# Kernel tuning notes

Hardware: AMD Instinct MI355X
Metric: run time of the kernel (lower is better)

The kernel has to match this reference:

```python
import jax, jax.numpy as jnp
import numpy as np

K = 32
START = K - 2  # index of <START>
STOP = K - 1   # index of <STOP>
NEG = -10000.0
B, T = 512, 2048


def setup_inputs() -> dict:
    key = jax.random.key(0)
    k1, k2, k3, k4 = jax.random.split(key, 4)
    feats = jax.random.normal(k1, (B, T, K), dtype=jnp.float32)
    transitions = jax.random.normal(k2, (K, K), dtype=jnp.float32)
    # constraints set in __init__: never transition TO START, never FROM STOP
    transitions = transitions.at[START, :].set(NEG).at[:, STOP].set(NEG)
    tags = jax.random.randint(k3, (B, T), 0, K - 2)          # real tags only
    lens = jnp.maximum(jax.random.randint(k4, (B,), 0, T), 1)  # at least 1 token
    return {"feats": feats, "transitions": transitions, "tags": tags, "lens": lens}


def _crf_loss(feats, transitions, tags, lens):
    Bn, Tn, Kn = feats.shape
    # ---- forward algorithm (log-partition) ----
    init = jnp.full((Bn, Kn), NEG, feats.dtype).at[:, START].set(0.0)

    def step(alpha, emit):
        # alpha[b,prev] + trans[next,prev] -> logsumexp over prev, then + emit[b,next]
        nxt = jax.scipy.special.logsumexp(
            alpha[:, None, :] + transitions[None, :, :], axis=2) + emit
        return nxt, nxt

    _, alphas = jax.lax.scan(step, init, jnp.swapaxes(feats, 0, 1))  # [T,B,K]
    alphas = jnp.concatenate([init[None], alphas], axis=0)           # [T+1,B,K]
    alpha_at_len = alphas[lens, jnp.arange(Bn)]                      # [B,K]
    forward_score = jax.scipy.special.logsumexp(
        alpha_at_len + transitions[STOP][None, :], axis=1)           # [B]

    # ---- gold score ----
    tags_stop = jnp.where(jnp.arange(Tn)[None, :] < lens[:, None], tags, STOP)
    pad_start = jnp.concatenate(
        [jnp.full((Bn, 1), START, tags.dtype), tags], axis=1)        # [B,T+1]
    pad_stop = jnp.concatenate(
        [tags_stop, jnp.full((Bn, 1), STOP, tags.dtype)], axis=1)    # [B,T+1]
    trans_mask = jnp.arange(Tn + 1)[None, :] <= lens[:, None]        # len+1 transitions
    trans_sc = jnp.where(trans_mask, transitions[pad_stop, pad_start], 0.0).sum(axis=1)
    emit_mask = jnp.arange(Tn)[None, :] < lens[:, None]
    emit_sc = jnp.where(
        emit_mask,
        jnp.take_along_axis(feats, tags[:, :, None], axis=2)[..., 0],
        0.0).sum(axis=1)
    gold_score = trans_sc + emit_sc

    return jnp.mean(forward_score - gold_score)


def reference(feats, transitions, tags, lens):
    return _crf_loss(feats, transitions, tags, lens)
```

## Files before the change

kernel.cpp:

```cpp
#include <hip/hip_runtime.h>
#include <hip/hip_bf16.h>
#include <cstdint>
#include <cstddef>

#define Kn 32
#define Bn 512
#define Tn 2048
#define CH 128
#define NC (Tn / CH)
#define GP 4
#define MMB (Bn * 2)
#define GB  Bn
#define START 30
#define STOP 31
#define LN2F 0.69314718055994530942f

typedef __attribute__((ext_vector_type(8))) short bf16x8;
typedef __attribute__((ext_vector_type(16))) float f32x16;
typedef __attribute__((ext_vector_type(2))) float f32x2;

union BF8 { bf16x8 v; unsigned u[4]; };

__device__ __forceinline__ unsigned pk2z(float lo, float hi) {
  return __builtin_amdgcn_perm(__float_as_uint(hi), __float_as_uint(lo),
                               0x07060302u);
}

__device__ __forceinline__ float bcast32(float v, int idx) {
  return __shfl(v, idx, 32);
}

__global__ __launch_bounds__(256, 4) void crf_fused(
    const float* __restrict__ feats, const float* __restrict__ trans,
    const int* __restrict__ tags, const int* __restrict__ lens,
    float* __restrict__ pmats, float* __restrict__ poffs,
    float* __restrict__ gold_part) {
  const int wid = threadIdx.x >> 6;
  const int lane = threadIdx.x & 63;

  if (blockIdx.x < MMB) {
    const int b = blockIdx.x >> 1;
    const int widx = (blockIdx.x & 1) * 4 + wid;
    const int len = lens[b];
    const int m = lane & 31;
    const int h = lane >> 5;

    f32x2 e1[4], e2[4];
    {
      const float* tr = trans + m * Kn + 8 * h;
#pragma unroll
      for (int j = 0; j < 4; ++j) {
        e1[j] = (f32x2){__expf(tr[2 * j]) * 0.0078125f,
                        __expf(tr[2 * j + 1]) * 0.0078125f};
        e2[j] = (f32x2){__expf(tr[16 + 2 * j]) * 0.0078125f,
                        __expf(tr[16 + 2 * j + 1]) * 0.0078125f};
      }
    }
    unsigned i1[4] = {0, 0, 0, 0}, i2[4] = {0, 0, 0, 0};
    {
      int j = m - 8 * h;
      if (0 <= j && j < 8) i1[j >> 1] = (j & 1) ? 0x3F800000u : 0x00003F80u;
      j = m - 16 - 8 * h;
      if (0 <= j && j < 8) i2[j >> 1] = (j & 1) ? 0x3F800000u : 0x00003F80u;
    }
    const f32x16 zf = {0.f, 0.f, 0.f, 0.f, 0.f, 0.f, 0.f, 0.f,
                       0.f, 0.f, 0.f, 0.f, 0.f, 0.f, 0.f, 0.f};

    for (int cc = 0; cc < 2; ++cc) {
      const int c = widx + cc * 8;
      const int nsteps = min(max(len - c * CH, 0), CH);
      if (nsteps == 0) break;

      unsigned b1u[4], b2u[4];
#pragma unroll
      for (int j = 0; j < 4; ++j) { b1u[j] = i1[j]; b2u[j] = i2[j]; }

      f32x16 acc;
      float off = 0.0f;
      const int t0 = c * CH;
      const float* fb = feats + ((size_t)b * Tn + t0) * Kn + m;
      const int lim = Tn - 1 - t0;

      float ring[8];
#pragma unroll
      for (int i = 0; i < 8; ++i) ring[i] = fb[(size_t)min(i, lim) * Kn];

      auto mmstep = [&](float f, bool rn) {
        const float w = __expf(f);
        const f32x2 w2 = {w, w};
        BF8 A1, A2, B1, B2;
#pragma unroll
        for (int j = 0; j < 4; ++j) {
          const f32x2 p1 = e1[j] * w2;
          const f32x2 p2 = e2[j] * w2;
          A1.u[j] = pk2z(p1.x, p1.y);
          A2.u[j] = pk2z(p2.x, p2.y);
          B1.u[j] = b1u[j];
          B2.u[j] = b2u[j];
        }
        acc = __builtin_amdgcn_mfma_f32_32x32x16_bf16(A2.v, B2.v, zf, 0, 0, 0);
        acc = __builtin_amdgcn_mfma_f32_32x32x16_bf16(A1.v, B1.v, acc, 0, 0, 0);

        if (rn) {
          float mx = acc[0];
#pragma unroll
          for (int r = 1; r < 16; ++r) mx = fmaxf(mx, acc[r]);
#pragma unroll
          for (int d = 1; d < 64; d <<= 1) mx = fmaxf(mx, __shfl_xor(mx, d));
          const int e = (int)((__float_as_uint(mx) >> 23) & 255u);
          const float sc = __uint_as_float((unsigned)(254 - e) << 23);
#pragma unroll
          for (int r = 0; r < 16; ++r) acc[r] *= sc;
          off += (float)(e - 127) * LN2F;
        }

        const unsigned qa = pk2z(acc[0], acc[1]);
        const unsigned qb = pk2z(acc[2], acc[3]);
        const unsigned qc = pk2z(acc[4], acc[5]);
        const unsigned qd = pk2z(acc[6], acc[7]);
        const unsigned qe = pk2z(acc[8], acc[9]);
        const unsigned qf = pk2z(acc[10], acc[11]);
        const unsigned qg = pk2z(acc[12], acc[13]);
        const unsigned qh = pk2z(acc[14], acc[15]);
        const unsigned ra = __shfl_xor(qa, 32);
        const unsigned rb = __shfl_xor(qb, 32);
        const unsigned rc = __shfl_xor(qc, 32);
        const unsigned rd = __shfl_xor(qd, 32);
        const unsigned re = __shfl_xor(qe, 32);
        const unsigned rf = __shfl_xor(qf, 32);
        const unsigned rg = __shfl_xor(qg, 32);
        const unsigned rh = __shfl_xor(qh, 32);
        b1u[0] = h ? rc : qa;
        b1u[1] = h ? rd : qb;
        b1u[2] = h ? qc : ra;
        b1u[3] = h ? qd : rb;
        b2u[0] = h ? rg : qe;
        b2u[1] = h ? rh : qf;
        b2u[2] = h ? qg : re;
        b2u[3] = h ? qh : rf;
      };

      int t = 0;
      const int nb = nsteps >> 3;
      for (int mb = 0; mb < nb; ++mb) {
#pragma unroll
        for (int i = 0; i < 8; ++i) {
          const float f = ring[i];
          ring[i] = fb[(size_t)min(t + i + 8, lim) * Kn];
          mmstep(f, ((t + i) & 31) == 31);
        }
        t += 8;
      }
      const int rem = nsteps & 7;
      for (int i = 0; i < rem; ++i) mmstep(ring[i], false);

      float* pm = pmats + (size_t)(b * NC + c) * (Kn * Kn);
#pragma unroll
      for (int r = 0; r < 16; ++r) {
        const int row = (r & 3) + 8 * (r >> 2) + 4 * h;
        pm[row * Kn + m] = acc[r];
      }
      if (lane == 0) poffs[b * NC + c] = off + 7.0f * LN2F * (float)nsteps;
    }
  } else {
    const int b = blockIdx.x - MMB;
    const int len = lens[b];
    const int* tg = tags + (size_t)b * Tn;
    const float* fbp = feats + (size_t)b * Tn * Kn;
    float acc = 0.f;
    for (int tt = 64 * wid + lane; tt < len; tt += 256) {
      const int tag = tg[tt];
      const int prev = tt ? tg[tt - 1] : START;
      acc += fbp[(size_t)tt * Kn + tag] + trans[tag * Kn + prev];
      if (tt == len - 1) acc += trans[STOP * Kn + tag];
    }
#pragma unroll
    for (int msk = 32; msk >= 1; msk >>= 1) acc += __shfl_xor(acc, msk);
    if (lane == 0) gold_part[b * GP + wid] = acc;
  }
}

__device__ __forceinline__ float renorm_s(float& s, float off) {
  int e = (int)((__float_as_uint(s) >> 23) & 255u);
  e = max(e, __shfl_xor(e, 1));
  e = max(e, __shfl_xor(e, 2));
  e = max(e, __shfl_xor(e, 4));
  e = max(e, __shfl_xor(e, 8));
  e = max(e, __shfl_xor(e, 16));
  s *= __uint_as_float((unsigned)(254 - e) << 23);
  return off + (float)(e - 127) * LN2F;
}

__global__ __launch_bounds__(64, 1) void crf_apply(
    const float* __restrict__ trans, const int* __restrict__ lens,
    const float* __restrict__ pmats, const float* __restrict__ poffs,
    const float* __restrict__ gold_part, float* __restrict__ out) {
  const int lane = threadIdx.x;
  const int b = blockIdx.x;
  const int n = lane & 31;
  const int hb = (lane >> 5) * 16;
  const int len = lens[b];
  const int nc = (len + CH - 1) / CH;
  float s = (n == START) ? 1.0f : 0.0f;
  float off = 0.0f;
  for (int c = 0; c < nc; ++c) {
    const float* pm = pmats + (size_t)(b * NC + c) * (Kn * Kn) + n * Kn + hb;
    const float4 p0 = *(const float4*)pm;
    const float4 p1 = *(const float4*)(pm + 4);
    const float4 p2 = *(const float4*)(pm + 8);
    const float4 p3 = *(const float4*)(pm + 12);
    float a0 = 0.f, a1 = 0.f, a2 = 0.f, a3 = 0.f;
    a0 = fmaf(bcast32(s, hb + 0), p0.x, a0);
    a0 = fmaf(bcast32(s, hb + 1), p0.y, a0);
    a0 = fmaf(bcast32(s, hb + 2), p0.z, a0);
    a0 = fmaf(bcast32(s, hb + 3), p0.w, a0);
    a1 = fmaf(bcast32(s, hb + 4), p1.x, a1);
    a1 = fmaf(bcast32(s, hb + 5), p1.y, a1);
    a1 = fmaf(bcast32(s, hb + 6), p1.z, a1);
    a1 = fmaf(bcast32(s, hb + 7), p1.w, a1);
    a2 = fmaf(bcast32(s, hb + 8), p2.x, a2);
    a2 = fmaf(bcast32(s, hb + 9), p2.y, a2);
    a2 = fmaf(bcast32(s, hb + 10), p2.z, a2);
    a2 = fmaf(bcast32(s, hb + 11), p2.w, a2);
    a3 = fmaf(bcast32(s, hb + 12), p3.x, a3);
    a3 = fmaf(bcast32(s, hb + 13), p3.y, a3);
    a3 = fmaf(bcast32(s, hb + 14), p3.z, a3);
    a3 = fmaf(bcast32(s, hb + 15), p3.w, a3);
    float p = (a0 + a1) + (a2 + a3);
    p += __shfl_xor(p, 32);
    s = p;
    off = renorm_s(s, off);
    off += poffs[b * NC + c];
  }
  const float es = __expf(trans[STOP * Kn + n]);
  float q = s * es;
#pragma unroll
  for (int d = 1; d < 32; d <<= 1) q += __shfl_xor(q, d);
  if (lane == 0) {
    const float fs = __logf(q) + off;
    float gs = 0.f;
#pragma unroll
    for (int p = 0; p < GP; ++p) gs += gold_part[b * GP + p];
    atomicAdd(out, (fs - gs) * (1.0f / (float)Bn));
  }
}

extern "C" void kernel_launch(void* const* d_in, const int* in_sizes, int n_in,
                              void* d_out, int out_size, void* d_ws, size_t ws_size,
                              hipStream_t stream) {
  const float* feats = (const float*)d_in[0];
  const float* trans = (const float*)d_in[1];
  const int* tags = (const int*)d_in[2];
  const int* lens = (const int*)d_in[3];

  float* gold_part = (float*)d_ws;
  float* poffs = gold_part + (size_t)Bn * GP;
  float* pmats = poffs + (size_t)Bn * NC;

  hipMemsetAsync(d_out, 0, (size_t)out_size * sizeof(float), stream);
  crf_fused<<<MMB + GB, 256, 0, stream>>>(feats, trans, tags, lens, pmats,
                                          poffs, gold_part);
  crf_apply<<<Bn, 64, 0, stream>>>(trans, lens, pmats, poffs, gold_part,
                                   (float*)d_out);
}
```

Baseline: 282.3 us.

## Interleave two adjacent chunk chains per wave and stage apply matrices in LDS

Each wave now processes two adjacent chunks (c0, c1) at once instead of two widely spaced chunks in sequence. Their MFMA dependency chains are interleaved so one chain's latency can hide the other's. Waves whose chunks lie entirely past the sequence length now exit early. The cross-half shuffles are replaced with v_permlane32_swap, and occupancy is lowered to 3 blocks to make room for the extra registers. The apply kernel now uses 256 threads to cooperatively load all chunk matrices into swizzled shared memory before a single wave runs the serial chain. This takes global-load latency off that serial chain, at the cost of a barrier and more LDS.

```diff
diff --git a/kernel.cpp b/kernel.cpp
--- a/kernel.cpp
+++ b/kernel.cpp
@@ -1,5 +1,4 @@
 #include <hip/hip_runtime.h>
-#include <hip/hip_bf16.h>
 #include <cstdint>
 #include <cstddef>
 
@@ -30,7 +29,20 @@
   return __shfl(v, idx, 32);
 }
 
-__global__ __launch_bounds__(256, 4) void crf_fused(
+__device__ __forceinline__ void plswap(unsigned& a, unsigned& b) {
+  asm("v_permlane32_swap_b32 %0, %1" : "+v"(a), "+v"(b));
+}
+
+struct Chain {
+  unsigned bu[8];
+  f32x16 acc;
+  float off;
+  float ring[8];
+  const float* fb;
+  int lim;
+};
+
+__global__ __launch_bounds__(256, 3) void crf_fused(
     const float* __restrict__ feats, const float* __restrict__ trans,
     const int* __restrict__ tags, const int* __restrict__ lens,
     float* __restrict__ pmats, float* __restrict__ poffs,
@@ -42,6 +54,11 @@
     const int b = blockIdx.x >> 1;
     const int widx = (blockIdx.x & 1) * 4 + wid;
     const int len = lens[b];
+    const int c0 = 2 * widx, c1 = c0 + 1;
+    const int n0 = min(max(len - c0 * CH, 0), CH);
+    const int n1 = min(max(len - c1 * CH, 0), CH);
+    if (n0 == 0) return;
+
     const int m = lane & 31;
     const int h = lane >> 5;
 
@@ -56,111 +73,122 @@
                         __expf(tr[16 + 2 * j + 1]) * 0.0078125f};
       }
     }
-    unsigned i1[4] = {0, 0, 0, 0}, i2[4] = {0, 0, 0, 0};
-    {
+    const f32x16 zf = {0.f, 0.f, 0.f, 0.f, 0.f, 0.f, 0.f, 0.f,
+                       0.f, 0.f, 0.f, 0.f, 0.f, 0.f, 0.f, 0.f};
+
+    auto init_chain = [&](Chain& ch, int c) {
+      unsigned i1[4] = {0, 0, 0, 0}, i2[4] = {0, 0, 0, 0};
       int j = m - 8 * h;
       if (0 <= j && j < 8) i1[j >> 1] = (j & 1) ? 0x3F800000u : 0x00003F80u;
       j = m - 16 - 8 * h;
       if (0 <= j && j < 8) i2[j >> 1] = (j & 1) ? 0x3F800000u : 0x00003F80u;
-    }
-    const f32x16 zf = {0.f, 0.f, 0.f, 0.f, 0.f, 0.f, 0.f, 0.f,
-                       0.f, 0.f, 0.f, 0.f, 0.f, 0.f, 0.f, 0.f};
-
-    for (int cc = 0; cc < 2; ++cc) {
-      const int c = widx + cc * 8;
-      const int nsteps = min(max(len - c * CH, 0), CH);
-      if (nsteps == 0) break;
-
-      unsigned b1u[4], b2u[4];
-#pragma unroll
-      for (int j = 0; j < 4; ++j) { b1u[j] = i1[j]; b2u[j] = i2[j]; }
-
-      f32x16 acc;
-      float off = 0.0f;
+#pragma unroll
+      for (int k = 0; k < 4; ++k) { ch.bu[k] = i1[k]; ch.bu[4 + k] = i2[k]; }
+      ch.off = 0.f;
       const int t0 = c * CH;
-      const float* fb = feats + ((size_t)b * Tn + t0) * Kn + m;
-      const int lim = Tn - 1 - t0;
-
-      float ring[8];
-#pragma unroll
-      for (int i = 0; i < 8; ++i) ring[i] = fb[(size_t)min(i, lim) * Kn];
-
-      auto mmstep = [&](float f, bool rn) {
-        const float w = __expf(f);
-        const f32x2 w2 = {w, w};
-        BF8 A1, A2, B1, B2;
-#pragma unroll
-        for (int j = 0; j < 4; ++j) {
-          const f32x2 p1 = e1[j] * w2;
-          const f32x2 p2 = e2[j] * w2;
-          A1.u[j] = pk2z(p1.x, p1.y);
-          A2.u[j] = pk2z(p2.x, p2.y);
-          B1.u[j] = b1u[j];
-          B2.u[j] = b2u[j];
-        }
-        acc = __builtin_amdgcn_mfma_f32_32x32x16_bf16(A2.v, B2.v, zf, 0, 0, 0);
-        acc = __builtin_amdgcn_mfma_f32_32x32x16_bf16(A1.v, B1.v, acc, 0, 0, 0);
-
-        if (rn) {
-          float mx = acc[0];
-#pragma unroll
-          for (int r = 1; r < 16; ++r) mx = fmaxf(mx, acc[r]);
-#pragma unroll
-          for (int d = 1; d < 64; d <<= 1) mx = fmaxf(mx, __shfl_xor(mx, d));
-          const int e = (int)((__float_as_uint(mx) >> 23) & 255u);
-          const float sc = __uint_as_float((unsigned)(254 - e) << 23);
-#pragma unroll
-          for (int r = 0; r < 16; ++r) acc[r] *= sc;
-          off += (float)(e - 127) * LN2F;
-        }
-
-        const unsigned qa = pk2z(acc[0], acc[1]);
-        const unsigned qb = pk2z(acc[2], acc[3]);
-        const unsigned qc = pk2z(acc[4], acc[5]);
-        const unsigned qd = pk2z(acc[6], acc[7]);
-        const unsigned qe = pk2z(acc[8], acc[9]);
-        const unsigned qf = pk2z(acc[10], acc[11]);
-        const unsigned qg = pk2z(acc[12], acc[13]);
-        const unsigned qh = pk2z(acc[14], acc[15]);
-        const unsigned ra = __shfl_xor(qa, 32);
-        const unsigned rb = __shfl_xor(qb, 32);
-        const unsigned rc = __shfl_xor(qc, 32);
-        const unsigned rd = __shfl_xor(qd, 32);
-        const unsigned re = __shfl_xor(qe, 32);
-        const unsigned rf = __shfl_xor(qf, 32);
-        const unsigned rg = __shfl_xor(qg, 32);
-        const unsigned rh = __shfl_xor(qh, 32);
-        b1u[0] = h ? rc : qa;
-        b1u[1] = h ? rd : qb;
-        b1u[2] = h ? qc : ra;
-        b1u[3] = h ? qd : rb;
-        b2u[0] = h ? rg : qe;
-        b2u[1] = h ? rh : qf;
-        b2u[2] = h ? qg : re;
-        b2u[3] = h ? qh : rf;
-      };
-
-      int t = 0;
-      const int nb = nsteps >> 3;
-      for (int mb = 0; mb < nb; ++mb) {
-#pragma unroll
-        for (int i = 0; i < 8; ++i) {
-          const float f = ring[i];
-          ring[i] = fb[(size_t)min(t + i + 8, lim) * Kn];
-          mmstep(f, ((t + i) & 31) == 31);
-        }
-        t += 8;
-      }
-      const int rem = nsteps & 7;
-      for (int i = 0; i < rem; ++i) mmstep(ring[i], false);
-
-      float* pm = pmats + (size_t)(b * NC + c) * (Kn * Kn);
+      ch.fb = feats + ((size_t)b * Tn + t0) * Kn + m;
+      ch.lim = Tn - 1 - t0;
+#pragma unroll
+      for (int i = 0; i < 8; ++i) ch.ring[i] = ch.fb[(size_t)min(i, ch.lim) * Kn];
+    };
+
+    auto mm = [&](Chain& ch, float f, bool rn) {
+      const float w = __expf(f);
+      const f32x2 w2 = {w, w};
+      BF8 A1, A2, B1, B2;
+#pragma unroll
+      for (int j = 0; j < 4; ++j) {
+        const f32x2 p1 = e1[j] * w2;
+        const f32x2 p2 = e2[j] * w2;
+        A1.u[j] = pk2z(p1.x, p1.y);
+        A2.u[j] = pk2z(p2.x, p2.y);
+        B1.u[j] = ch.bu[j];
+        B2.u[j] = ch.bu[4 + j];
+      }
+      f32x16 acc = __builtin_amdgcn_mfma_f32_32x32x16_bf16(A2.v, B2.v, zf, 0, 0, 0);
+      acc = __builtin_amdgcn_mfma_f32_32x32x16_bf16(A1.v, B1.v, acc, 0, 0, 0);
+
+      if (rn) {
+        float mx = acc[0];
+#pragma unroll
+        for (int r = 1; r < 16; ++r) mx = fmaxf(mx, acc[r]);
+#pragma unroll
+        for (int d = 1; d < 64; d <<= 1) mx = fmaxf(mx, __shfl_xor(mx, d));
+        const int e = (int)((__float_as_uint(mx) >> 23) & 255u);
+        const float sc = __uint_as_float((unsigned)(254 - e) << 23);
+#pragma unroll
+        for (int r = 0; r < 16; ++r) acc[r] *= sc;
+        ch.off += (float)(e - 127) * LN2F;
+      }
+
+      unsigned qa = pk2z(acc[0], acc[1]);
+      unsigned qb = pk2z(acc[2], acc[3]);
+      unsigned qc = pk2z(acc[4], acc[5]);
+      unsigned qd = pk2z(acc[6], acc[7]);
+      unsigned qe = pk2z(acc[8], acc[9]);
+      unsigned qf = pk2z(acc[10], acc[11]);
+      unsigned qg = pk2z(acc[12], acc[13]);
+      unsigned qh = pk2z(acc[14], acc[15]);
+      plswap(qa, qc);
+      plswap(qb, qd);
+      plswap(qe, qg);
+      plswap(qf, qh);
+      ch.bu[0] = qa; ch.bu[1] = qb; ch.bu[2] = qc; ch.bu[3] = qd;
+      ch.bu[4] = qe; ch.bu[5] = qf; ch.bu[6] = qg; ch.bu[7] = qh;
+      ch.acc = acc;
+    };
+
+    Chain ch0, ch1;
+    init_chain(ch0, c0);
+    if (n1) init_chain(ch1, c1);
+
+    const int nb0 = n0 >> 3;
+    const int nb1 = n1 >> 3;
+    int t = 0;
+    for (int mb = 0; mb < nb1; ++mb) {
+#pragma unroll
+      for (int i = 0; i < 8; ++i) {
+        const float f0 = ch0.ring[i];
+        ch0.ring[i] = ch0.fb[(size_t)min(t + i + 8, ch0.lim) * Kn];
+        const float f1 = ch1.ring[i];
+        ch1.ring[i] = ch1.fb[(size_t)min(t + i + 8, ch1.lim) * Kn];
+        const bool rn = ((t + i) & 31) == 31;
+        mm(ch0, f0, rn);
+        mm(ch1, f1, rn);
+      }
+      t += 8;
+    }
+    for (int mb = nb1; mb < nb0; ++mb) {
+#pragma unroll
+      for (int i = 0; i < 8; ++i) {
+        const float f0 = ch0.ring[i];
+        ch0.ring[i] = ch0.fb[(size_t)min(t + i + 8, ch0.lim) * Kn];
+        mm(ch0, f0, ((t + i) & 31) == 31);
+      }
+      t += 8;
+    }
+    const int r0 = n0 & 7;
+    for (int i = 0; i < r0; ++i) mm(ch0, ch0.ring[i], false);
+    const int r1 = n1 & 7;
+    for (int i = 0; i < r1; ++i) mm(ch1, ch1.ring[i], false);
+
+    {
+      float* pm = pmats + (size_t)(b * NC + c0) * (Kn * Kn);
 #pragma unroll
       for (int r = 0; r < 16; ++r) {
         const int row = (r & 3) + 8 * (r >> 2) + 4 * h;
-        pm[row * Kn + m] = acc[r];
-      }
-      if (lane == 0) poffs[b * NC + c] = off + 7.0f * LN2F * (float)nsteps;
+        pm[row * Kn + m] = ch0.acc[r];
+      }
+      if (lane == 0) poffs[b * NC + c0] = ch0.off + 7.0f * LN2F * (float)n0;
+    }
+    if (n1) {
+      float* pm = pmats + (size_t)(b * NC + c1) * (Kn * Kn);
+#pragma unroll
+      for (int r = 0; r < 16; ++r) {
+        const int row = (r & 3) + 8 * (r >> 2) + 4 * h;
+        pm[row * Kn + m] = ch1.acc[r];
+      }
+      if (lane == 0) poffs[b * NC + c1] = ch1.off + 7.0f * LN2F * (float)n1;
     }
   } else {
     const int b = blockIdx.x - MMB;
@@ -191,24 +219,38 @@
   return off + (float)(e - 127) * LN2F;
 }
 
-__global__ __launch_bounds__(64, 1) void crf_apply(
+__global__ __launch_bounds__(256, 2) void crf_apply(
     const float* __restrict__ trans, const int* __restrict__ lens,
     const float* __restrict__ pmats, const float* __restrict__ poffs,
     const float* __restrict__ gold_part, float* __restrict__ out) {
-  const int lane = threadIdx.x;
+  __shared__ float4 smat[NC * 256];
+  const int tid = threadIdx.x;
   const int b = blockIdx.x;
+  const int len = lens[b];
+  const int nc = (len + CH - 1) / CH;
+
+  const float4* gp = (const float4*)(pmats + (size_t)b * NC * (Kn * Kn));
+  for (int qq = tid; qq < nc * 256; qq += 256) {
+    const int row = (qq >> 3) & 31;
+    const int g = qq & 7;
+    smat[(qq & ~7) | (g ^ (row & 7))] = gp[qq];
+  }
+  __syncthreads();
+  if (tid >= 64) return;
+
+  const int lane = tid;
   const int n = lane & 31;
   const int hb = (lane >> 5) * 16;
-  const int len = lens[b];
-  const int nc = (len + CH - 1) / CH;
+  const int g0 = hb >> 2;
+  const int nsw = n & 7;
   float s = (n == START) ? 1.0f : 0.0f;
   float off = 0.0f;
   for (int c = 0; c < nc; ++c) {
-    const float* pm = pmats + (size_t)(b * NC + c) * (Kn * Kn) + n * Kn + hb;
-    const float4 p0 = *(const float4*)pm;
-    const float4 p1 = *(const float4*)(pm + 4);
-    const float4 p2 = *(const float4*)(pm + 8);
-    const float4 p3 = *(const float4*)(pm + 12);
+    const float4* mr = &smat[(c << 8) | (n << 3)];
+    const float4 p0 = mr[(g0 + 0) ^ nsw];
+    const float4 p1 = mr[(g0 + 1) ^ nsw];
+    const float4 p2 = mr[(g0 + 2) ^ nsw];
+    const float4 p3 = mr[(g0 + 3) ^ nsw];
     float a0 = 0.f, a1 = 0.f, a2 = 0.f, a3 = 0.f;
     a0 = fmaf(bcast32(s, hb + 0), p0.x, a0);
     a0 = fmaf(bcast32(s, hb + 1), p0.y, a0);
@@ -240,7 +282,7 @@
     const float fs = __logf(q) + off;
     float gs = 0.f;
 #pragma unroll
-    for (int p = 0; p < GP; ++p) gs += gold_part[b * GP + p];
+    for (int gi = 0; gi < GP; ++gi) gs += gold_part[b * GP + gi];
     atomicAdd(out, (fs - gs) * (1.0f / (float)Bn));
   }
 }
@@ -260,6 +302,6 @@
   hipMemsetAsync(d_out, 0, (size_t)out_size * sizeof(float), stream);
   crf_fused<<<MMB + GB, 256, 0, stream>>>(feats, trans, tags, lens, pmats,
                                           poffs, gold_part);
-  crf_apply<<<Bn, 64, 0, stream>>>(trans, lens, pmats, poffs, gold_part,
-                                   (float*)d_out);
-}
+  crf_apply<<<Bn, 256, 0, stream>>>(trans, lens, pmats, poffs, gold_part,
+                                    (float*)d_out);
+}
```

Result: no change. 286.0 us (+1.3%).
